# Kernel tuning notes

Hardware: AMD Instinct MI355X
Metric: run time of the kernel (lower is better)

The kernel has to match this reference:

```python
import jax, jax.numpy as jnp
import numpy as np

V, N, H, A_DIM, F_OUT = 3, 8192, 128, 64, 128


def setup_inputs() -> dict:
    key = jax.random.key(0)
    ks = jax.random.split(key, 13)
    s = 0.02
    w = lambda k, shape: jax.random.normal(k, shape, jnp.float32) * s
    adj = jax.random.randint(ks[0], (V, N, N), 0, 2, dtype=jnp.int32)
    return {
        "adjacency_matrices_list": adj,
        "W1": w(ks[1], (V, N, H)), "b1": w(ks[2], (V, H)),
        "W2": w(ks[3], (V, H, H)), "b2": w(ks[4], (V, H)),
        "Wa1": w(ks[5], (H, A_DIM)), "ba1": w(ks[6], (A_DIM,)),
        "Wa2": w(ks[7], (A_DIM, 1)), "ba2": w(ks[8], (1,)),
        "Wf1": w(ks[9], (H * V, 2 * H)), "bf1": w(ks[10], (2 * H,)),
        "Wf2": w(ks[11], (2 * H, F_OUT)), "bf2": w(ks[12], (F_OUT,)),
    }


def _norm_adj(adj_int):
    # PyG GCNConv gcn_norm on binary edges: add remaining self-loops, then D^-1/2 (A+I) D^-1/2
    a = (adj_int != 0).astype(jnp.float32)            # (V,N,N) binary
    eye = jnp.eye(adj_int.shape[-1], dtype=jnp.float32)
    ah = a * (1.0 - eye) + eye                        # force diagonal to exactly 1
    dinv = jax.lax.rsqrt(ah.sum(-1))                  # deg >= 1, safe
    return ah * dinv[..., :, None] * dinv[..., None, :]


def _forward(adj, W1, b1, W2, b2, Wa1, ba1, Wa2, ba2, Wf1, bf1, Wf2, bf2):
    A = _norm_adj(adj)                                # (V,N,N)
    # initial features X = eye(N), so A @ (X @ W1) == A @ W1
    h = jax.nn.relu(jnp.einsum('vnm,vmh->vnh', A, W1) + b1[:, None, :])
    h = jnp.einsum('vnh,vhk->vnk', h, W2)
    h = jax.nn.relu(jnp.einsum('vnm,vmk->vnk', A, h) + b2[:, None, :])  # (V,N,H) view embeddings
    # attention fusion
    summ = h.mean(axis=1)                             # (V,H) view summaries
    scores = (jnp.tanh(summ @ Wa1 + ba1) @ Wa2 + ba2)[:, 0]
    attn = jax.nn.softmax(scores, axis=0)             # (V,)
    weighted = h * attn[:, None, None]
    fusion_in = jnp.transpose(weighted, (1, 0, 2)).reshape(h.shape[1], -1)  # (N, V*H)
    fused = jax.nn.relu(fusion_in @ Wf1 + bf1) @ Wf2 + bf2                  # (N, F_OUT)
    return fused, attn, h


def reference(adjacency_matrices_list, W1, b1, W2, b2, Wa1, ba1, Wa2, ba2, Wf1, bf1, Wf2, bf2):
    return _forward(adjacency_matrices_list, W1, b1, W2, b2, Wa1, ba1, Wa2, ba2, Wf1, bf1, Wf2, bf2)
```

## Files before the change

kernel.cpp:

```cpp
#include <hip/hip_runtime.h>
#include <hip/hip_bf16.h>

#define VV 3
#define NN 8192
#define HH 128
#define ADIM 64
#define FOUT 128

typedef short bf16x8 __attribute__((ext_vector_type(8)));
typedef float f32x4 __attribute__((ext_vector_type(4)));
typedef unsigned char uchar;

__device__ __forceinline__ float bf2f(ushort u) {
    union { unsigned int i; float f; } x; x.i = ((unsigned int)u) << 16; return x.f;
}
__device__ __forceinline__ ushort f2bf(float f) {
    union { float f; unsigned int i; } x; x.f = f;
    unsigned int r = (x.i + 0x7FFFu + ((x.i >> 16) & 1u)) >> 16;
    return (ushort)r;
}
__device__ __forceinline__ void async_cp16(const void* g, void* l) {
    __builtin_amdgcn_global_load_lds(
        (const __attribute__((address_space(1))) void*)g,
        (__attribute__((address_space(3))) void*)l, 16, 0, 0);
}

__global__ void zero_k(float* p, int n) {
    int i = blockIdx.x * blockDim.x + threadIdx.x;
    if (i < n) p[i] = 0.0f;
}

__global__ __launch_bounds__(256) void pack_k(const int* __restrict__ adj,
                                              uchar* __restrict__ abits,
                                              float* __restrict__ dinv) {
    const int t = threadIdx.x;
    const int r = t >> 1, half = t & 1;
    const int mt = blockIdx.x, z = blockIdx.y;
    const int n = mt * 128 + r;
    const long rowoff = ((long)z * NN + n) * NN;
    uint* dst = (uint*)(abits + (((long)z * 64 + mt) * 128 << 10));
    int cnt = 0;
    for (int kc = 0; kc < 128; kc++) {
        const int colbase = kc * 64 + half * 32;
        uint wbits = 0;
        #pragma unroll
        for (int i = 0; i < 8; i++) {
            const int c0 = colbase + i * 4;
            const int4 v = *(const int4*)(adj + rowoff + c0);
            uint b0 = (v.x != 0 || c0 + 0 == n) ? 1u : 0u;
            uint b1 = (v.y != 0 || c0 + 1 == n) ? 1u : 0u;
            uint b2 = (v.z != 0 || c0 + 2 == n) ? 1u : 0u;
            uint b3 = (v.w != 0 || c0 + 3 == n) ? 1u : 0u;
            wbits |= (b0 | (b1 << 1) | (b2 << 2) | (b3 << 3)) << (i * 4);
        }
        cnt += __popc(wbits);
        dst[kc * 256 + t] = wbits;
    }
    cnt += __shfl_xor(cnt, 1);
    if (half == 0) dinv[(long)z * NN + n] = rsqrtf((float)cnt);
}

template<int INF32>
__global__ void transpose_scale_k(const void* __restrict__ in_, ushort* __restrict__ out,
                                  int R, int C, const float* __restrict__ scale, int scale_z) {
    __shared__ ushort tile[32][33];
    const long zo = (long)blockIdx.z * R * C;
    const int c0 = blockIdx.x * 32, r0 = blockIdx.y * 32;
    const int t = threadIdx.x;
    #pragma unroll
    for (int p = 0; p < 4; p++) {
        int e = p * 256 + t; int row = e >> 5, col = e & 31;
        long idx = zo + (long)(r0 + row) * C + c0 + col;
        float x = INF32 ? ((const float*)in_)[idx] : bf2f(((const ushort*)in_)[idx]);
        if (scale) x *= scale[(long)blockIdx.z * scale_z + r0 + row];
        tile[row][col] = f2bf(x);
    }
    __syncthreads();
    #pragma unroll
    for (int p = 0; p < 4; p++) {
        int e = p * 256 + t; int row = e >> 5, col = e & 31;
        out[zo + (long)(c0 + row) * R + r0 + col] = tile[col][row];
    }
}

template<int WRITE_F32>
__global__ __launch_bounds__(128) void gemm_adj_k(
    const uchar* __restrict__ abits,
    const ushort* __restrict__ Bt,
    const float* __restrict__ dinv,
    const float* __restrict__ bias,
    ushort* __restrict__ hout,
    float* __restrict__ fout)
{
    __shared__ __align__(16) uchar As[512];
    __shared__ __align__(16) ushort Bs[128 * 64];
    const int tid = threadIdx.x, lane = tid & 63, wc = tid >> 6;
    const int mt = blockIdx.x, z = blockIdx.y;
    const int m0 = mt * 64;
    const uchar* Achunks = abits + (((long)z * 64 + (mt >> 1)) * 128 << 10);
    const int arow_off = (mt & 1) * 512;
    const ushort* Bv = Bt + (long)z * 128 * NN;
    f32x4 acc[4][4] = {};

    int srow[8], slcb[8];
    #pragma unroll
    for (int p = 0; p < 8; p++) {
        int slot = p * 128 + tid;
        srow[p] = slot >> 3;
        slcb[p] = (slot & 7) ^ (srow[p] & 7);
    }

    for (int kc = 0; kc < 128; kc++) {
        if (tid < 32)
            async_cp16(Achunks + ((long)kc << 10) + arow_off + tid * 16, As + tid * 16);
        const int k0 = kc * 64;
        #pragma unroll
        for (int p = 0; p < 8; p++) {
            const int slot = p * 128 + tid;
            async_cp16(Bv + (long)srow[p] * NN + k0 + slcb[p] * 8, Bs + slot * 8);
        }
        __syncthreads();
        const int q = lane >> 4;
        uint2 bitsarr[4];
        #pragma unroll
        for (int mi = 0; mi < 4; mi++)
            bitsarr[mi] = *(const uint2*)&As[(mi * 16 + (lane & 15)) * 8];
        #pragma unroll
        for (int s = 0; s < 2; s++) {
            bf16x8 bb[4];
            const int ca = s * 4 + q;
            #pragma unroll
            for (int ni = 0; ni < 4; ni++) {
                int r = wc * 64 + ni * 16 + (lane & 15);
                bb[ni] = *(const bf16x8*)&Bs[r * 64 + ((ca ^ (r & 7)) * 8)];
            }
            #pragma unroll
            for (int mi = 0; mi < 4; mi++) {
                const uint wsel = s ? bitsarr[mi].y : bitsarr[mi].x;
                const uint b = (wsel >> (q * 8)) & 0xffu;
                union { uint4 u; bf16x8 v; } cvt;
                cvt.u.x = ((b     ) & 1u) * 0x00003F80u | ((b >> 1) & 1u) * 0x3F800000u;
                cvt.u.y = ((b >> 2) & 1u) * 0x00003F80u | ((b >> 3) & 1u) * 0x3F800000u;
                cvt.u.z = ((b >> 4) & 1u) * 0x00003F80u | ((b >> 5) & 1u) * 0x3F800000u;
                cvt.u.w = ((b >> 6) & 1u) * 0x00003F80u | ((b >> 7) & 1u) * 0x3F800000u;
                #pragma unroll
                for (int ni = 0; ni < 4; ni++)
                    acc[mi][ni] = __builtin_amdgcn_mfma_f32_16x16x32_bf16(cvt.v, bb[ni], acc[mi][ni], 0, 0, 0);
            }
        }
        __syncthreads();
    }

    const long zo = (long)z * NN * HH;
    #pragma unroll
    for (int mi = 0; mi < 4; mi++) {
        int rbase = m0 + mi * 16 + ((lane >> 4) << 2);
        #pragma unroll
        for (int ni = 0; ni < 4; ni++) {
            int col = wc * 64 + ni * 16 + (lane & 15);
            float bcol = bias[z * HH + col];
            #pragma unroll
            for (int r = 0; r < 4; r++) {
                int grow = rbase + r;
                float v = fmaxf(acc[mi][ni][r] * dinv[(long)z * NN + grow] + bcol, 0.0f);
                hout[zo + (long)grow * HH + col] = f2bf(v);
                if (WRITE_F32) fout[zo + (long)grow * HH + col] = v;
            }
        }
    }
}

template<int AMODE, int EPI, int OUTF32>
__global__ __launch_bounds__(256) void gemm_k(
    const void* __restrict__ Aany, long a_zs, int lda,
    const ushort* __restrict__ Bt, long b_zs, int ldb,
    void* __restrict__ Cc, long c_zs, int ldc,
    int Ktot,
    const float* __restrict__ dinv, int dinv_zs,
    const float* __restrict__ bias, int bias_zs,
    const float* __restrict__ attnp)
{
    __shared__ __align__(16) ushort As[128][40];
    __shared__ __align__(16) ushort Bs[128][40];
    const int tid = threadIdx.x;
    const int bx = blockIdx.x, by = blockIdx.y, z = blockIdx.z;
    const int m0 = by * 128, n0 = bx * 128;
    const int lane = tid & 63, w = tid >> 6, wr = w >> 1, wcq = w & 1;
    f32x4 acc[4][4] = {};
    float att0 = 0.f, att1 = 0.f, att2 = 0.f;
    if (AMODE == 2) { att0 = attnp[0]; att1 = attnp[1]; att2 = attnp[2]; }
    const ushort* Ab = (const ushort*)Aany + (long)z * (AMODE == 1 ? a_zs : 0);
    const ushort* Btz = Bt + (long)z * b_zs;

    for (int k0 = 0; k0 < Ktot; k0 += 32) {
        if (AMODE == 1) {
            #pragma unroll
            for (int p = 0; p < 2; p++) {
                int c = p * 256 + tid;
                int row = c >> 2, q = c & 3;
                *(int4*)&As[row][q * 8] = *(const int4*)(Ab + (long)(m0 + row) * lda + k0 + q * 8);
            }
        } else {
            #pragma unroll
            for (int p = 0; p < 2; p++) {
                int c = p * 256 + tid;
                int row = c >> 2, q = c & 3;
                int kk = k0 + q * 8;
                int v = kk >> 7, ko = kk & 127;
                int4 raw = *(const int4*)((const ushort*)Aany + (long)v * a_zs + (long)(m0 + row) * HH + ko);
                float sc = (v == 0) ? att0 : (v == 1 ? att1 : att2);
                __align__(16) ushort us[8];
                *(int4*)us = raw;
                #pragma unroll
                for (int e = 0; e < 8; e++) us[e] = f2bf(bf2f(us[e]) * sc);
                *(int4*)&As[row][q * 8] = *(int4*)us;
            }
        }
        #pragma unroll
        for (int p = 0; p < 2; p++) {
            int c = p * 256 + tid;
            int n = c >> 2, q = c & 3;
            *(int4*)&Bs[n][q * 8] = *(const int4*)(Btz + (long)(n0 + n) * ldb + k0 + q * 8);
        }
        __syncthreads();
        bf16x8 af[4], bfr[4];
        #pragma unroll
        for (int mi = 0; mi < 4; mi++)
            af[mi] = *(const bf16x8*)&As[wr * 64 + mi * 16 + (lane & 15)][(lane >> 4) * 8];
        #pragma unroll
        for (int ni = 0; ni < 4; ni++)
            bfr[ni] = *(const bf16x8*)&Bs[wcq * 64 + ni * 16 + (lane & 15)][(lane >> 4) * 8];
        #pragma unroll
        for (int mi = 0; mi < 4; mi++)
            #pragma unroll
            for (int ni = 0; ni < 4; ni++)
                acc[mi][ni] = __builtin_amdgcn_mfma_f32_16x16x32_bf16(af[mi], bfr[ni], acc[mi][ni], 0, 0, 0);
        __syncthreads();
    }

    #pragma unroll
    for (int mi = 0; mi < 4; mi++) {
        int rbase = m0 + wr * 64 + mi * 16 + ((lane >> 4) << 2);
        #pragma unroll
        for (int ni = 0; ni < 4; ni++) {
            int col = n0 + wcq * 64 + ni * 16 + (lane & 15);
            #pragma unroll
            for (int r = 0; r < 4; r++) {
                int grow = rbase + r;
                float vv = acc[mi][ni][r];
                if (EPI == 1) vv *= dinv[(long)z * dinv_zs + grow];
                if (EPI == 2 || EPI == 3) vv += bias[col];
                if (EPI == 2) vv = fmaxf(vv, 0.0f);
                if (OUTF32) ((float*)Cc + (long)z * c_zs)[(long)grow * ldc + col] = vv;
                else        ((ushort*)Cc + (long)z * c_zs)[(long)grow * ldc + col] = f2bf(vv);
            }
        }
    }
}

__global__ __launch_bounds__(256) void colsum_k(const ushort* __restrict__ h2,
                                                float* __restrict__ summ) {
    const int rowbase = blockIdx.x * 64;
    const int z = rowbase >> 13;
    const int col = threadIdx.x & 127, half = threadIdx.x >> 7;
    float s = 0.0f;
    for (int r = half; r < 64; r += 2) s += bf2f(h2[(long)(rowbase + r) * HH + col]);
    atomicAdd(&summ[z * HH + col], s);
}

__global__ __launch_bounds__(256) void attn_k(const float* __restrict__ summ,
                                              const float* __restrict__ Wa1,
                                              const float* __restrict__ ba1,
                                              const float* __restrict__ Wa2,
                                              const float* __restrict__ ba2,
                                              float* __restrict__ attnws,
                                              float* __restrict__ out_attn) {
    __shared__ float sc[VV];
    const int tid = threadIdx.x;
    if (tid < VV * 64) {
        const int v = tid >> 6, a = tid & 63;
        float s = ba1[a];
        const float invN = 1.0f / (float)NN;
        #pragma unroll 4
        for (int h = 0; h < HH; h++) s += summ[v * HH + h] * invN * Wa1[h * ADIM + a];
        float p = tanhf(s) * Wa2[a];
        for (int off = 32; off; off >>= 1) p += __shfl_down(p, off);
        if (a == 0) sc[v] = p + ba2[0];
    }
    __syncthreads();
    if (tid == 0) {
        float m = fmaxf(sc[0], fmaxf(sc[1], sc[2]));
        float e0 = expf(sc[0] - m), e1 = expf(sc[1] - m), e2 = expf(sc[2] - m);
        float inv = 1.0f / (e0 + e1 + e2);
        attnws[0] = e0 * inv; attnws[1] = e1 * inv; attnws[2] = e2 * inv;
        out_attn[0] = e0 * inv; out_attn[1] = e1 * inv; out_attn[2] = e2 * inv;
    }
}

extern "C" void kernel_launch(void* const* d_in, const int* in_sizes, int n_in,
                              void* d_out, int out_size, void* d_ws, size_t ws_size,
                              hipStream_t stream) {
    const int*   adj = (const int*)d_in[0];
    const float* W1  = (const float*)d_in[1];
    const float* b1  = (const float*)d_in[2];
    const float* W2  = (const float*)d_in[3];
    const float* b2  = (const float*)d_in[4];
    const float* Wa1 = (const float*)d_in[5];
    const float* ba1 = (const float*)d_in[6];
    const float* Wa2 = (const float*)d_in[7];
    const float* ba2 = (const float*)d_in[8];
    const float* Wf1 = (const float*)d_in[9];
    const float* bf1 = (const float*)d_in[10];
    const float* Wf2 = (const float*)d_in[11];
    const float* bf2v = (const float*)d_in[12];

    float* out = (float*)d_out;
    float* out_fused = out;
    float* out_attn  = out + (long)NN * FOUT;
    float* out_h     = out + (long)NN * FOUT + VV;

    char* wsb = (char*)d_ws;
    const long SZ_DINV  = (long)VV * NN * 4;
    const long SZ_ABITS = (long)VV * 64 * 128 * 1024;
    const long SZ_W1T   = (long)VV * HH * NN * 2;
    const long SZ_W2T   = (long)VV * HH * HH * 2;
    const long SZ_WF1T  = 256L * 384 * 2;
    const long SZ_WF2T  = 128L * 256 * 2;
    const long SZ_VNH   = (long)VV * NN * HH * 2;
    const long SZ_G     = (long)NN * 256 * 2;
    long off = 0;
    float*  dinv  = (float*)(wsb + off);  off += SZ_DINV;
    uchar*  abits = (uchar*)(wsb + off);  off += SZ_ABITS;
    ushort* w1t   = (ushort*)(wsb + off); off += SZ_W1T;
    ushort* w2t   = (ushort*)(wsb + off); off += SZ_W2T;
    ushort* wf1t  = (ushort*)(wsb + off); off += SZ_WF1T;
    ushort* wf2t  = (ushort*)(wsb + off); off += SZ_WF2T;
    ushort* h1    = (ushort*)(wsb + off); off += SZ_VNH;
    ushort* tbuf  = (ushort*)(wsb + off); off += SZ_VNH;
    ushort* tT    = (ushort*)(wsb + off); off += SZ_VNH;
    ushort* h2    = (ushort*)(wsb + off); off += SZ_VNH;
    ushort* G     = (ushort*)(wsb + off); off += SZ_G;
    float*  summ  = (float*)(wsb + off);  off += 1600;
    float*  attnw = summ + 384;

    const long VNH = (long)NN * HH;

    zero_k<<<2, 256, 0, stream>>>(summ, 400);
    pack_k<<<dim3(64, VV), 256, 0, stream>>>(adj, abits, dinv);
    transpose_scale_k<1><<<dim3(4, 256, VV), 256, 0, stream>>>(W1, w1t, NN, HH, dinv, NN);
    transpose_scale_k<1><<<dim3(4, 4, VV), 256, 0, stream>>>(W2, w2t, HH, HH, nullptr, 0);
    transpose_scale_k<1><<<dim3(8, 12, 1), 256, 0, stream>>>(Wf1, wf1t, 384, 256, nullptr, 0);
    transpose_scale_k<1><<<dim3(4, 8, 1), 256, 0, stream>>>(Wf2, wf2t, 256, 128, nullptr, 0);
    gemm_adj_k<0><<<dim3(128, VV), 128, 0, stream>>>(abits, w1t, dinv, b1, h1, nullptr);
    gemm_k<1, 1, 0><<<dim3(1, 64, VV), 256, 0, stream>>>(h1, VNH, HH, w2t, (long)HH * HH, HH,
                                                         tbuf, VNH, HH, HH, dinv, NN, nullptr, 0, nullptr);
    transpose_scale_k<0><<<dim3(4, 256, VV), 256, 0, stream>>>(tbuf, tT, NN, HH, nullptr, 0);
    gemm_adj_k<1><<<dim3(128, VV), 128, 0, stream>>>(abits, tT, dinv, b2, h2, out_h);
    colsum_k<<<(VV * NN) / 64, 256, 0, stream>>>(h2, summ);
    attn_k<<<1, 256, 0, stream>>>(summ, Wa1, ba1, Wa2, ba2, attnw, out_attn);
    gemm_k<2, 2, 0><<<dim3(2, 64, 1), 256, 0, stream>>>(h2, VNH, HH, wf1t, 0, 384,
                                                        G, 0, 256, 384, nullptr, 0, bf1, 0, attnw);
    gemm_k<1, 3, 1><<<dim3(1, 64, 1), 256, 0, stream>>>(G, 0, 256, wf2t, 0, 256,
                                                        out_fused, 0, FOUT, 256, nullptr, 0, bf2v, 0, nullptr);
}
```

Baseline: 1.542 ms.

## Split adjacency packing over column halves and widen adjacency GEMM to four waves

The adjacency pack kernel is split across two column halves, so the grid doubles from 192 to 384 blocks. Row degrees are now accumulated with atomics into a zeroed int buffer, and a new small kernel converts them to inverse square roots. The adjacency GEMM moves from 2 to 4 waves per block in a 2x2 wave grid, with each wave covering 32 rows instead of 64, which lowers per-wave accumulator registers and spreads the B-tile loads. The pack kernel reading 800MB of int adjacency likely dominates, and 192 blocks may underfill the GPU, so the extra parallelism targets that cost at the price of atomics and an extra launch.

```diff
diff --git a/kernel.cpp b/kernel.cpp
--- a/kernel.cpp
+++ b/kernel.cpp
@@ -32,15 +32,15 @@
 
 __global__ __launch_bounds__(256) void pack_k(const int* __restrict__ adj,
                                               uchar* __restrict__ abits,
-                                              float* __restrict__ dinv) {
+                                              int* __restrict__ deg) {
     const int t = threadIdx.x;
     const int r = t >> 1, half = t & 1;
-    const int mt = blockIdx.x, z = blockIdx.y;
+    const int ks = blockIdx.x, mt = blockIdx.y, z = blockIdx.z;
     const int n = mt * 128 + r;
     const long rowoff = ((long)z * NN + n) * NN;
     uint* dst = (uint*)(abits + (((long)z * 64 + mt) * 128 << 10));
     int cnt = 0;
-    for (int kc = 0; kc < 128; kc++) {
+    for (int kc = ks * 64; kc < ks * 64 + 64; kc++) {
         const int colbase = kc * 64 + half * 32;
         uint wbits = 0;
         #pragma unroll
@@ -54,10 +54,15 @@
             wbits |= (b0 | (b1 << 1) | (b2 << 2) | (b3 << 3)) << (i * 4);
         }
         cnt += __popc(wbits);
-        dst[kc * 256 + t] = wbits;
+        dst[kc * 256 + r * 2 + half] = wbits;
     }
     cnt += __shfl_xor(cnt, 1);
-    if (half == 0) dinv[(long)z * NN + n] = rsqrtf((float)cnt);
+    if (half == 0) atomicAdd(&deg[z * NN + n], cnt);
+}
+
+__global__ void dinv_k(const int* __restrict__ deg, float* __restrict__ dinv) {
+    int i = blockIdx.x * blockDim.x + threadIdx.x;
+    if (i < VV * NN) dinv[i] = rsqrtf((float)deg[i]);
 }
 
 template<int INF32>
@@ -84,7 +89,7 @@
 }
 
 template<int WRITE_F32>
-__global__ __launch_bounds__(128) void gemm_adj_k(
+__global__ __launch_bounds__(256) void gemm_adj_k(
     const uchar* __restrict__ abits,
     const ushort* __restrict__ Bt,
     const float* __restrict__ dinv,
@@ -94,18 +99,19 @@
 {
     __shared__ __align__(16) uchar As[512];
     __shared__ __align__(16) ushort Bs[128 * 64];
-    const int tid = threadIdx.x, lane = tid & 63, wc = tid >> 6;
+    const int tid = threadIdx.x, lane = tid & 63, w = tid >> 6;
+    const int wrow = w >> 1, wcol = w & 1;
     const int mt = blockIdx.x, z = blockIdx.y;
     const int m0 = mt * 64;
     const uchar* Achunks = abits + (((long)z * 64 + (mt >> 1)) * 128 << 10);
     const int arow_off = (mt & 1) * 512;
     const ushort* Bv = Bt + (long)z * 128 * NN;
-    f32x4 acc[4][4] = {};
-
-    int srow[8], slcb[8];
-    #pragma unroll
-    for (int p = 0; p < 8; p++) {
-        int slot = p * 128 + tid;
+    f32x4 acc[2][4] = {};
+
+    int srow[4], slcb[4];
+    #pragma unroll
+    for (int p = 0; p < 4; p++) {
+        int slot = p * 256 + tid;
         srow[p] = slot >> 3;
         slcb[p] = (slot & 7) ^ (srow[p] & 7);
     }
@@ -115,27 +121,27 @@
             async_cp16(Achunks + ((long)kc << 10) + arow_off + tid * 16, As + tid * 16);
         const int k0 = kc * 64;
         #pragma unroll
-        for (int p = 0; p < 8; p++) {
-            const int slot = p * 128 + tid;
+        for (int p = 0; p < 4; p++) {
+            const int slot = p * 256 + tid;
             async_cp16(Bv + (long)srow[p] * NN + k0 + slcb[p] * 8, Bs + slot * 8);
         }
         __syncthreads();
         const int q = lane >> 4;
-        uint2 bitsarr[4];
-        #pragma unroll
-        for (int mi = 0; mi < 4; mi++)
-            bitsarr[mi] = *(const uint2*)&As[(mi * 16 + (lane & 15)) * 8];
+        uint2 bitsarr[2];
+        #pragma unroll
+        for (int mi = 0; mi < 2; mi++)
+            bitsarr[mi] = *(const uint2*)&As[(wrow * 32 + mi * 16 + (lane & 15)) * 8];
         #pragma unroll
         for (int s = 0; s < 2; s++) {
             bf16x8 bb[4];
             const int ca = s * 4 + q;
             #pragma unroll
             for (int ni = 0; ni < 4; ni++) {
-                int r = wc * 64 + ni * 16 + (lane & 15);
-                bb[ni] = *(const bf16x8*)&Bs[r * 64 + ((ca ^ (r & 7)) * 8)];
-            }
-            #pragma unroll
-            for (int mi = 0; mi < 4; mi++) {
+                int brow = wcol * 64 + ni * 16 + (lane & 15);
+                bb[ni] = *(const bf16x8*)&Bs[brow * 64 + ((ca ^ (brow & 7)) * 8)];
+            }
+            #pragma unroll
+            for (int mi = 0; mi < 2; mi++) {
                 const uint wsel = s ? bitsarr[mi].y : bitsarr[mi].x;
                 const uint b = (wsel >> (q * 8)) & 0xffu;
                 union { uint4 u; bf16x8 v; } cvt;
@@ -153,11 +159,11 @@
 
     const long zo = (long)z * NN * HH;
     #pragma unroll
-    for (int mi = 0; mi < 4; mi++) {
-        int rbase = m0 + mi * 16 + ((lane >> 4) << 2);
+    for (int mi = 0; mi < 2; mi++) {
+        int rbase = m0 + wrow * 32 + mi * 16 + ((lane >> 4) << 2);
         #pragma unroll
         for (int ni = 0; ni < 4; ni++) {
-            int col = wc * 64 + ni * 16 + (lane & 15);
+            int col = wcol * 64 + ni * 16 + (lane & 15);
             float bcol = bias[z * HH + col];
             #pragma unroll
             for (int r = 0; r < 4; r++) {
@@ -342,20 +348,22 @@
     ushort* G     = (ushort*)(wsb + off); off += SZ_G;
     float*  summ  = (float*)(wsb + off);  off += 1600;
     float*  attnw = summ + 384;
+    int*    deg   = (int*)(wsb + off);    off += (long)VV * NN * 4;
 
     const long VNH = (long)NN * HH;
 
-    zero_k<<<2, 256, 0, stream>>>(summ, 400);
-    pack_k<<<dim3(64, VV), 256, 0, stream>>>(adj, abits, dinv);
+    zero_k<<<98, 256, 0, stream>>>(summ, 400 + VV * NN);
+    pack_k<<<dim3(2, 64, VV), 256, 0, stream>>>(adj, abits, deg);
+    dinv_k<<<96, 256, 0, stream>>>(deg, dinv);
     transpose_scale_k<1><<<dim3(4, 256, VV), 256, 0, stream>>>(W1, w1t, NN, HH, dinv, NN);
     transpose_scale_k<1><<<dim3(4, 4, VV), 256, 0, stream>>>(W2, w2t, HH, HH, nullptr, 0);
     transpose_scale_k<1><<<dim3(8, 12, 1), 256, 0, stream>>>(Wf1, wf1t, 384, 256, nullptr, 0);
     transpose_scale_k<1><<<dim3(4, 8, 1), 256, 0, stream>>>(Wf2, wf2t, 256, 128, nullptr, 0);
-    gemm_adj_k<0><<<dim3(128, VV), 128, 0, stream>>>(abits, w1t, dinv, b1, h1, nullptr);
+    gemm_adj_k<0><<<dim3(128, VV), 256, 0, stream>>>(abits, w1t, dinv, b1, h1, nullptr);
     gemm_k<1, 1, 0><<<dim3(1, 64, VV), 256, 0, stream>>>(h1, VNH, HH, w2t, (long)HH * HH, HH,
                                                          tbuf, VNH, HH, HH, dinv, NN, nullptr, 0, nullptr);
     transpose_scale_k<0><<<dim3(4, 256, VV), 256, 0, stream>>>(tbuf, tT, NN, HH, nullptr, 0);
-    gemm_adj_k<1><<<dim3(128, VV), 128, 0, stream>>>(abits, tT, dinv, b2, h2, out_h);
+    gemm_adj_k<1><<<dim3(128, VV), 256, 0, stream>>>(abits, tT, dinv, b2, h2, out_h);
     colsum_k<<<(VV * NN) / 64, 256, 0, stream>>>(h2, summ);
     attn_k<<<1, 256, 0, stream>>>(summ, Wa1, ba1, Wa2, ba2, attnw, out_attn);
     gemm_k<2, 2, 0><<<dim3(2, 64, 1), 256, 0, stream>>>(h2, VNH, HH, wf1t, 0, 384,
```

New measurement: 1.584 ms. +2.7%, slower.
